# Optimization experiments

Hardware: AMD Instinct MI355X
Metric: run time of the kernel (lower is better)

The kernel has to match this reference:

```python
import jax, jax.numpy as jnp
import numpy as np

B, H, S, D = 2, 16, 2048, 64


def setup_inputs() -> dict:
    key = jax.random.key(0)
    kq, kk, kv, km = jax.random.split(key, 4)
    q = jax.random.normal(kq, (B, H, S, D), dtype=jnp.float32)
    k = jax.random.normal(kk, (B, H, S, D), dtype=jnp.float32)
    v = jax.random.normal(kv, (B, H, S, D), dtype=jnp.float32)
    mask = jax.random.uniform(km, (B, H, S, S), dtype=jnp.float32)
    return {"q": q, "k": k, "v": v, "mask": mask}


def reference(q, k, v, mask):
    # qk: [B,H,S,S]
    qk = jnp.einsum("bhqd,bhkd->bhqk", q, k)
    qkm = qk * mask
    # abs-sum-clamp normalizer; original uses .detach() -> stop_gradient
    r = jnp.sum(jnp.abs(qkm), axis=-1, keepdims=True)
    r = jnp.maximum(jax.lax.stop_gradient(r), 1.0)
    o = jnp.einsum("bhqk,bhkd->bhqd", qkm / r, v)
    return o
```

## Files before the change

### kernel.cpp

```cpp
#include <hip/hip_runtime.h>

#define S_LEN 2048
#define DHEAD 64
#define TQ 64
#define TK 64
#define NIT (S_LEN / TK)
#define BH 32

typedef __attribute__((ext_vector_type(4))) short short4v;
typedef __attribute__((ext_vector_type(8))) short short8v;
typedef __attribute__((ext_vector_type(4))) float float4v;
typedef __attribute__((ext_vector_type(2))) int int2v;
typedef __attribute__((ext_vector_type(4))) int int4v;

__device__ __forceinline__ unsigned bfr(float x) {
    return __builtin_bit_cast(unsigned, x) + 0x8000u;
}
__device__ __forceinline__ int packbf(float a, float b) {
    return (int)((bfr(a) >> 16) | (bfr(b) & 0xFFFF0000u));
}

__global__ __launch_bounds__(256, 4)
void fra_kernel(const float* __restrict__ qg, const float* __restrict__ kg,
                const float* __restrict__ vg, const float* __restrict__ mg,
                float* __restrict__ og) {
    const int tid = threadIdx.x;
    const int l  = tid & 63;
    const int w  = tid >> 6;
    const int lg = l >> 4;
    const int ln = l & 15;
    const int q0 = blockIdx.x * TQ;
    const int bh = blockIdx.y;

    __shared__ __align__(16) short Kt[64 * 72];
    __shared__ __align__(16) short Vt[64 * 72];

    const float* qbase = qg + (size_t)bh * S_LEN * DHEAD;
    const float* kbase = kg + (size_t)bh * S_LEN * DHEAD;
    const float* vbase = vg + (size_t)bh * S_LEN * DHEAD;
    const float* mrow  = mg + (size_t)bh * S_LEN * S_LEN
                            + (size_t)(q0 + 16 * w + ln) * S_LEN;
    float*       obase = og + (size_t)bh * S_LEN * DHEAD;

    const int qrow = q0 + 16 * w + ln;
    short4v qf[4];
    #pragma unroll
    for (int s = 0; s < 4; ++s) {
        float4v qv = *(const float4v*)(qbase + (size_t)qrow * DHEAD + 16 * s + 4 * lg);
        int2v t; t.x = packbf(qv.x, qv.y); t.y = packbf(qv.z, qv.w);
        qf[s] = __builtin_bit_cast(short4v, t);
    }

    float4v oacc[4] = {{0.f,0.f,0.f,0.f},{0.f,0.f,0.f,0.f},
                       {0.f,0.f,0.f,0.f},{0.f,0.f,0.f,0.f}};
    float rpart = 0.f;

    const int sr = tid >> 4;
    const int sc = (tid & 15) * 4;

    const float* kptr = kbase + (size_t)sr * DHEAD + sc;
    const float* vptr = vbase + (size_t)(16 * w) * DHEAD + l;
    const float* mptr = mrow + 4 * lg;

    for (int it = 0; it < NIT; ++it) {
        float4v kv[4];
        #pragma unroll
        for (int p = 0; p < 4; ++p)
            kv[p] = *(const float4v*)(kptr + (size_t)(16 * p) * DHEAD);
        float vv[16];
        #pragma unroll
        for (int i = 0; i < 16; ++i)
            vv[i] = vptr[(size_t)i * DHEAD];
        float4v mf[4];
        #pragma unroll
        for (int mt = 0; mt < 4; ++mt)
            mf[mt] = *(const float4v*)(mptr + 16 * mt);

        kptr += TK * DHEAD; vptr += TK * DHEAD; mptr += TK;

        __syncthreads();

        #pragma unroll
        for (int p = 0; p < 4; ++p) {
            int2v t; t.x = packbf(kv[p].x, kv[p].y); t.y = packbf(kv[p].z, kv[p].w);
            *(short4v*)&Kt[(sr + 16 * p) * 72 + sc] = __builtin_bit_cast(short4v, t);
        }
        {
            int4v t0, t1;
            t0.x = packbf(vv[0], vv[1]);   t0.y = packbf(vv[2], vv[3]);
            t0.z = packbf(vv[4], vv[5]);   t0.w = packbf(vv[6], vv[7]);
            t1.x = packbf(vv[8], vv[9]);   t1.y = packbf(vv[10], vv[11]);
            t1.z = packbf(vv[12], vv[13]); t1.w = packbf(vv[14], vv[15]);
            *(short8v*)&Vt[l * 72 + 16 * w]     = __builtin_bit_cast(short8v, t0);
            *(short8v*)&Vt[l * 72 + 16 * w + 8] = __builtin_bit_cast(short8v, t1);
        }
        __syncthreads();

        #pragma unroll
        for (int mt = 0; mt < 4; ++mt) {
            float4v c1 = {0.f, 0.f, 0.f, 0.f};
            #pragma unroll
            for (int s = 0; s < 4; ++s) {
                short4v a1 = *(const short4v*)&Kt[(16 * mt + ln) * 72 + 16 * s + 4 * lg];
                c1 = __builtin_amdgcn_mfma_f32_16x16x16bf16_1k(a1, qf[s], c1, 0, 0, 0);
            }
            float p0 = c1.x * mf[mt].x;
            float p1 = c1.y * mf[mt].y;
            float p2 = c1.z * mf[mt].z;
            float p3 = c1.w * mf[mt].w;
            rpart += fabsf(p0) + fabsf(p1) + fabsf(p2) + fabsf(p3);
            int2v t; t.x = packbf(p0, p1); t.y = packbf(p2, p3);
            short4v a2 = __builtin_bit_cast(short4v, t);
            #pragma unroll
            for (int nt = 0; nt < 4; ++nt) {
                short4v b2 = *(const short4v*)&Vt[(16 * nt + ln) * 72 + 16 * mt + 4 * lg];
                oacc[nt] = __builtin_amdgcn_mfma_f32_16x16x16bf16_1k(a2, b2, oacc[nt], 0, 0, 0);
            }
        }
    }

    float r = rpart;
    r += __shfl_xor(r, 16);
    r += __shfl_xor(r, 32);

    #pragma unroll
    for (int reg = 0; reg < 4; ++reg) {
        float rq  = __shfl(r, 4 * lg + reg);
        float inv = 1.0f / fmaxf(rq, 1.0f);
        const int orow = q0 + 16 * w + 4 * lg + reg;
        #pragma unroll
        for (int nt = 0; nt < 4; ++nt) {
            obase[(size_t)orow * DHEAD + 16 * nt + ln] = oacc[nt][reg] * inv;
        }
    }
}

extern "C" void kernel_launch(void* const* d_in, const int* in_sizes, int n_in,
                              void* d_out, int out_size, void* d_ws, size_t ws_size,
                              hipStream_t stream) {
    const float* q = (const float*)d_in[0];
    const float* k = (const float*)d_in[1];
    const float* v = (const float*)d_in[2];
    const float* m = (const float*)d_in[3];
    float* o = (float*)d_out;
    (void)in_sizes; (void)n_in; (void)out_size; (void)d_ws; (void)ws_size;
    dim3 grid(S_LEN / TQ, BH);
    fra_kernel<<<grid, dim3(256, 1, 1), 0, stream>>>(q, k, v, m, o);
}
```

Measured before the change: 758.2 us.

## Double-buffer K/V shared tiles and prefetch next tile during MFMA compute

Adds two LDS buffers for K and V and a register double buffer for the mask fragments. The next tile's global loads are issued before the current tile's compute, and the bf16 stores into LDS follow it, leaving one barrier per iteration instead of two. This is meant to hide global memory latency behind matrix work, at the cost of twice the LDS and more live registers, which may lower occupancy.

```diff
diff --git a/kernel.cpp b/kernel.cpp
--- a/kernel.cpp
+++ b/kernel.cpp
@@ -32,8 +32,8 @@
     const int q0 = blockIdx.x * TQ;
     const int bh = blockIdx.y;
 
-    __shared__ __align__(16) short Kt[64 * 72];
-    __shared__ __align__(16) short Vt[64 * 72];
+    __shared__ __align__(16) short Kt[2][64 * 72];
+    __shared__ __align__(16) short Vt[2][64 * 72];
 
     const float* qbase = qg + (size_t)bh * S_LEN * DHEAD;
     const float* kbase = kg + (size_t)bh * S_LEN * DHEAD;
@@ -62,7 +62,9 @@
     const float* vptr = vbase + (size_t)(16 * w) * DHEAD + l;
     const float* mptr = mrow + 4 * lg;
 
-    for (int it = 0; it < NIT; ++it) {
+    float4v mfa[4], mfb[4];
+
+    {
         float4v kv[4];
         #pragma unroll
         for (int p = 0; p < 4; ++p)
@@ -71,29 +73,44 @@
         #pragma unroll
         for (int i = 0; i < 16; ++i)
             vv[i] = vptr[(size_t)i * DHEAD];
-        float4v mf[4];
         #pragma unroll
         for (int mt = 0; mt < 4; ++mt)
-            mf[mt] = *(const float4v*)(mptr + 16 * mt);
-
+            mfa[mt] = *(const float4v*)(mptr + 16 * mt);
         kptr += TK * DHEAD; vptr += TK * DHEAD; mptr += TK;
-
-        __syncthreads();
 
         #pragma unroll
         for (int p = 0; p < 4; ++p) {
             int2v t; t.x = packbf(kv[p].x, kv[p].y); t.y = packbf(kv[p].z, kv[p].w);
-            *(short4v*)&Kt[(sr + 16 * p) * 72 + sc] = __builtin_bit_cast(short4v, t);
+            *(short4v*)&Kt[0][(sr + 16 * p) * 72 + sc] = __builtin_bit_cast(short4v, t);
         }
-        {
-            int4v t0, t1;
-            t0.x = packbf(vv[0], vv[1]);   t0.y = packbf(vv[2], vv[3]);
-            t0.z = packbf(vv[4], vv[5]);   t0.w = packbf(vv[6], vv[7]);
-            t1.x = packbf(vv[8], vv[9]);   t1.y = packbf(vv[10], vv[11]);
-            t1.z = packbf(vv[12], vv[13]); t1.w = packbf(vv[14], vv[15]);
-            *(short8v*)&Vt[l * 72 + 16 * w]     = __builtin_bit_cast(short8v, t0);
-            *(short8v*)&Vt[l * 72 + 16 * w + 8] = __builtin_bit_cast(short8v, t1);
+        int4v t0, t1;
+        t0.x = packbf(vv[0], vv[1]);   t0.y = packbf(vv[2], vv[3]);
+        t0.z = packbf(vv[4], vv[5]);   t0.w = packbf(vv[6], vv[7]);
+        t1.x = packbf(vv[8], vv[9]);   t1.y = packbf(vv[10], vv[11]);
+        t1.z = packbf(vv[12], vv[13]); t1.w = packbf(vv[14], vv[15]);
+        *(short8v*)&Vt[0][l * 72 + 16 * w]     = __builtin_bit_cast(short8v, t0);
+        *(short8v*)&Vt[0][l * 72 + 16 * w + 8] = __builtin_bit_cast(short8v, t1);
+    }
+
+    auto iter_body = [&](int it, const short* KC, const short* VC,
+                         short* KN, short* VN,
+                         float4v* MC, float4v* MN) {
+        const bool hn = (it + 1 < NIT);
+        float4v kv[4];
+        float vv[16];
+        if (hn) {
+            #pragma unroll
+            for (int p = 0; p < 4; ++p)
+                kv[p] = *(const float4v*)(kptr + (size_t)(16 * p) * DHEAD);
+            #pragma unroll
+            for (int i = 0; i < 16; ++i)
+                vv[i] = vptr[(size_t)i * DHEAD];
+            #pragma unroll
+            for (int mt = 0; mt < 4; ++mt)
+                MN[mt] = *(const float4v*)(mptr + 16 * mt);
+            kptr += TK * DHEAD; vptr += TK * DHEAD; mptr += TK;
         }
+
         __syncthreads();
 
         #pragma unroll
@@ -101,22 +118,43 @@
             float4v c1 = {0.f, 0.f, 0.f, 0.f};
             #pragma unroll
             for (int s = 0; s < 4; ++s) {
-                short4v a1 = *(const short4v*)&Kt[(16 * mt + ln) * 72 + 16 * s + 4 * lg];
+                short4v a1 = *(const short4v*)&KC[(16 * mt + ln) * 72 + 16 * s + 4 * lg];
                 c1 = __builtin_amdgcn_mfma_f32_16x16x16bf16_1k(a1, qf[s], c1, 0, 0, 0);
             }
-            float p0 = c1.x * mf[mt].x;
-            float p1 = c1.y * mf[mt].y;
-            float p2 = c1.z * mf[mt].z;
-            float p3 = c1.w * mf[mt].w;
+            float p0 = c1.x * MC[mt].x;
+            float p1 = c1.y * MC[mt].y;
+            float p2 = c1.z * MC[mt].z;
+            float p3 = c1.w * MC[mt].w;
             rpart += fabsf(p0) + fabsf(p1) + fabsf(p2) + fabsf(p3);
             int2v t; t.x = packbf(p0, p1); t.y = packbf(p2, p3);
             short4v a2 = __builtin_bit_cast(short4v, t);
             #pragma unroll
             for (int nt = 0; nt < 4; ++nt) {
-                short4v b2 = *(const short4v*)&Vt[(16 * nt + ln) * 72 + 16 * mt + 4 * lg];
+                short4v b2 = *(const short4v*)&VC[(16 * nt + ln) * 72 + 16 * mt + 4 * lg];
                 oacc[nt] = __builtin_amdgcn_mfma_f32_16x16x16bf16_1k(a2, b2, oacc[nt], 0, 0, 0);
             }
         }
+
+        if (hn) {
+            #pragma unroll
+            for (int p = 0; p < 4; ++p) {
+                int2v t; t.x = packbf(kv[p].x, kv[p].y); t.y = packbf(kv[p].z, kv[p].w);
+                *(short4v*)&KN[(sr + 16 * p) * 72 + sc] = __builtin_bit_cast(short4v, t);
+            }
+            int4v t0, t1;
+            t0.x = packbf(vv[0], vv[1]);   t0.y = packbf(vv[2], vv[3]);
+            t0.z = packbf(vv[4], vv[5]);   t0.w = packbf(vv[6], vv[7]);
+            t1.x = packbf(vv[8], vv[9]);   t1.y = packbf(vv[10], vv[11]);
+            t1.z = packbf(vv[12], vv[13]); t1.w = packbf(vv[14], vv[15]);
+            *(short8v*)&VN[l * 72 + 16 * w]     = __builtin_bit_cast(short8v, t0);
+            *(short8v*)&VN[l * 72 + 16 * w + 8] = __builtin_bit_cast(short8v, t1);
+        }
+    };
+
+    #pragma unroll 1
+    for (int it2 = 0; it2 < NIT / 2; ++it2) {
+        iter_body(2 * it2,     Kt[0], Vt[0], Kt[1], Vt[1], mfa, mfb);
+        iter_body(2 * it2 + 1, Kt[1], Vt[1], Kt[0], Vt[0], mfb, mfa);
     }
 
     float r = rpart;
```

New measurement: 867.7 us. 14.4% more time.
